# Performance work log

Measured on AMD Instinct MI355X. Metric: run time of the kernel, lower is better.

## Reference

```python
import jax, jax.numpy as jnp
import numpy as np

D = 85  # label-distribution length -> selects A3 branch

def _build_A(d):
    if d == 5:
        base = jnp.arange(5)
        return 1.0 - jnp.abs(base[:, None] - base[None, :]) / 5.0
    if d == 10:
        base = jnp.arange(10)
        return 1.0 - jnp.abs(base[:, None] - base[None, :]) / 10.0
    base = jnp.arange(85)
    return (1.0 - jnp.abs(base[:, None] - base[None, :]) / 85.0).astype(jnp.float32)

def setup_inputs() -> dict:
    key = jax.random.key(0)
    k1, k2 = jax.random.split(key)
    B = 262144
    inp = jax.random.normal(k1, (B, D), dtype=jnp.float32)
    tgt = jax.random.uniform(k2, (B, D), dtype=jnp.float32)
    return {"input": inp, "target": tgt}

def reference(input, target):
    A = _build_A(input.shape[1]).astype(input.dtype)
    diff = jnp.abs(input - target)            # [B, d]
    # per-row quadratic form diff_i^T A diff_i, summed over batch
    q = jnp.einsum('bi,ij,bj->b', diff, A, diff)
    return 0.1 * q.sum()
```

## Files before the change

### kernel.cpp

```cpp
#include <hip/hip_runtime.h>


#define QFD_D 85
#define ROWS_PER_BLOCK 16
#define THREADS 64

#define F4_VALID 340
#define ROUNDS 6
#define BUF_FLOATS (ROUNDS * 256)

typedef __attribute__((address_space(1))) const void glob_cv;
typedef __attribute__((address_space(3))) void lds_v;

__global__ __launch_bounds__(THREADS) void qfd_kernel(
    const float* __restrict__ in, const float* __restrict__ tgt,
    float* __restrict__ partial) {
    __shared__ float lin[BUF_FLOATS];
    __shared__ float ltg[BUF_FLOATS];
    const int lane = threadIdx.x;
    const long base4 = (long)blockIdx.x * F4_VALID;

    const float4* in4 = reinterpret_cast<const float4*>(in) + base4;
    const float4* tg4 = reinterpret_cast<const float4*>(tgt) + base4;

    #pragma unroll
    for (int r = 0; r < ROUNDS; ++r) {
        int idx = r * 64 + lane;
        int g = idx < F4_VALID ? idx : 0;
        __builtin_amdgcn_global_load_lds(
            (glob_cv*)(in4 + g), (lds_v*)&lin[r * 256], 16, 0, 0);
        __builtin_amdgcn_global_load_lds(
            (glob_cv*)(tg4 + g), (lds_v*)&ltg[r * 256], 16, 0, 0);
    }
    __syncthreads();

    const int q   = lane & 3;
    const int row = lane >> 2;
    const int off = 21 * q + (q != 0);
    const int p   = row * QFD_D + off;

    float l = 0.0f, a1 = 0.0f, b2 = 0.0f;
    #pragma unroll
    for (int j = 0; j < 21; ++j) {
        float v = fabsf(lin[p + j] - ltg[p + j]);
        l += v;
        a1 += l;
        b2 = fmaf(l, l, b2);
    }
    if (q == 0) {
        float v = fabsf(lin[p + 21] - ltg[p + 21]);
        l += v;
        a1 += l;
        b2 = fmaf(l, l, b2);
    }

    const int qb = lane & 60;
    float s0 = __shfl(l, qb + 0, 64);
    float s1 = __shfl(l, qb + 1, 64);
    float s2 = __shfl(l, qb + 2, 64);
    float s3 = __shfl(l, qb + 3, 64);
    float S  = (s0 + s1) + (s2 + s3);
    float P  = (q > 0 ? s0 : 0.0f) + (q > 1 ? s1 : 0.0f) + (q > 2 ? s2 : 0.0f);
    float len = (q == 0) ? 22.0f : 21.0f;
    float c1 = fmaf(len, P, a1);
    float c2 = fmaf(len * P, P, fmaf(2.0f * P, a1, b2));
    float c1s = __shfl(c1, qb + 0, 64) + __shfl(c1, qb + 1, 64)
              + __shfl(c1, qb + 2, 64) + __shfl(c1, qb + 3, 64);
    float c2s = __shfl(c2, qb + 0, 64) + __shfl(c2, qb + 1, 64)
              + __shfl(c2, qb + 2, 64) + __shfl(c2, qb + 3, 64);
    float sumL  = c1s - S;
    float sumL2 = c2s - S * S;
    float qrow  = fmaf(S, S, -(2.0f / 85.0f) * (S * sumL - sumL2));
    float val   = (q == 0) ? qrow : 0.0f;

    #pragma unroll
    for (int m = 32; m > 0; m >>= 1)
        val += __shfl_xor(val, m, 64);
    if (lane == 0) partial[blockIdx.x] = val;
}

__global__ __launch_bounds__(256) void qfd_reduce_kernel(
    const float* __restrict__ partial, float* __restrict__ out, int n) {
    __shared__ float wsum[4];
    const int tid = threadIdx.x;
    float s = 0.0f;
    for (int i = tid; i < n; i += 256) s += partial[i];
    #pragma unroll
    for (int m = 32; m > 0; m >>= 1)
        s += __shfl_xor(s, m, 64);
    if ((tid & 63) == 0) wsum[tid >> 6] = s;
    __syncthreads();
    if (tid == 0) {
        float t = 0.0f;
        #pragma unroll
        for (int w = 0; w < 4; ++w) t += wsum[w];
        out[0] = 0.1f * t;
    }
}

extern "C" void kernel_launch(void* const* d_in, const int* in_sizes, int n_in,
                              void* d_out, int out_size, void* d_ws, size_t ws_size,
                              hipStream_t stream) {
    const float* in  = (const float*)d_in[0];
    const float* tgt = (const float*)d_in[1];
    float* out = (float*)d_out;
    float* partial = (float*)d_ws;

    const int B = in_sizes[0] / QFD_D;
    const int grid = B / ROWS_PER_BLOCK;

    qfd_kernel<<<grid, THREADS, 0, stream>>>(in, tgt, partial);
    qfd_reduce_kernel<<<1, 256, 0, stream>>>(partial, out, grid);
}
```

Before: 204.4 us.

## Replace LDS staging with direct register loads and grid-stride wave scans

Drops the global-to-LDS staging and instead has each wave read three 85-float rows straight into registers as unaligned 4-float vectors, with one extra scalar load for the row tail. Per-row prefix sums and the quadratic-form terms are built with full-wave shuffle scans. A fixed grid of 256-thread blocks runs a grid-stride loop over row groups, and a block-level reduction produces the partials. This removes the LDS round trip and the per-block launch overhead of many tiny blocks, at the cost of unaligned vector loads, a wasted lane per wave, and more shuffle work per row.

```diff
diff --git a/kernel.cpp b/kernel.cpp
--- a/kernel.cpp
+++ b/kernel.cpp
@@ -2,81 +2,118 @@
 
 
 #define QFD_D 85
-#define ROWS_PER_BLOCK 16
-#define THREADS 64
+#define THREADS 256
+#define NWAVES (THREADS / 64)
 
-#define F4_VALID 340
-#define ROUNDS 6
-#define BUF_FLOATS (ROUNDS * 256)
+typedef float f4a __attribute__((ext_vector_type(4), aligned(4)));
 
-typedef __attribute__((address_space(1))) const void glob_cv;
-typedef __attribute__((address_space(3))) void lds_v;
+__global__ __launch_bounds__(THREADS, 6) void qfd_kernel(
+    const float* __restrict__ in, const float* __restrict__ tgt,
+    float* __restrict__ partial, int B, int ngroups) {
+    __shared__ float wsum[NWAVES];
+    const int tid  = threadIdx.x;
+    const int lane = tid & 63;
+    const int wave = tid >> 6;
 
-__global__ __launch_bounds__(THREADS) void qfd_kernel(
-    const float* __restrict__ in, const float* __restrict__ tgt,
-    float* __restrict__ partial) {
-    __shared__ float lin[BUF_FLOATS];
-    __shared__ float ltg[BUF_FLOATS];
-    const int lane = threadIdx.x;
-    const long base4 = (long)blockIdx.x * F4_VALID;
+    const int r = (lane < 21) ? 0 : (lane < 42) ? 1 : (lane < 63) ? 2 : 3;
+    const int c = lane - 21 * r;
+    const bool isC20 = (c == 20) && (r < 3);
+    const int limv = B * QFD_D - 4;
+    const int lims = B * QFD_D - 1;
 
-    const float4* in4 = reinterpret_cast<const float4*>(in) + base4;
-    const float4* tg4 = reinterpret_cast<const float4*>(tgt) + base4;
+    const int wid     = blockIdx.x * NWAVES + wave;
+    const int wstride = gridDim.x * NWAVES;
 
-    #pragma unroll
-    for (int r = 0; r < ROUNDS; ++r) {
-        int idx = r * 64 + lane;
-        int g = idx < F4_VALID ? idx : 0;
-        __builtin_amdgcn_global_load_lds(
-            (glob_cv*)(in4 + g), (lds_v*)&lin[r * 256], 16, 0, 0);
-        __builtin_amdgcn_global_load_lds(
-            (glob_cv*)(tg4 + g), (lds_v*)&ltg[r * 256], 16, 0, 0);
+    float acc = 0.0f;
+
+    for (int g = wid; g < ngroups; g += wstride) {
+        const int base = g * 255;
+        const int row  = 3 * g + r;
+        const bool valid = (r < 3) && (row < B);
+
+        int off = base + r * 85 + c * 4;
+        off = off > limv ? limv : off;
+        f4a vi = *(const f4a*)(in  + off);
+        f4a vt = *(const f4a*)(tgt + off);
+
+        float ti = 0.0f, tt = 0.0f;
+        if (isC20) {
+            int toff = base + r * 85 + 84;
+            toff = toff > lims ? lims : toff;
+            ti = in[toff];
+            tt = tgt[toff];
+        }
+
+        float d0 = valid ? fabsf(vi.x - vt.x) : 0.0f;
+        float d1 = valid ? fabsf(vi.y - vt.y) : 0.0f;
+        float d2 = valid ? fabsf(vi.z - vt.z) : 0.0f;
+        float d3 = valid ? fabsf(vi.w - vt.w) : 0.0f;
+
+        float l  = d0;
+        float a1 = l;
+        float b2 = l * l;
+        l += d1; a1 += l; b2 = fmaf(l, l, b2);
+        l += d2; a1 += l; b2 = fmaf(l, l, b2);
+        l += d3; a1 += l; b2 = fmaf(l, l, b2);
+        const bool ct = isC20 && valid;
+        float d4 = ct ? fabsf(ti - tt) : 0.0f;
+        float l5 = l + d4;
+        a1 += ct ? l5 : 0.0f;
+        b2 = ct ? fmaf(l5, l5, b2) : b2;
+        l  = ct ? l5 : l;
+        float s = l;
+
+        float ps = s;
+        #pragma unroll
+        for (int d = 1; d < 64; d <<= 1) {
+            float t = __shfl_up(ps, d, 64);
+            if (lane >= d) ps += t;
+        }
+        float bs1 = __shfl(ps, 20, 64);
+        float bs2 = __shfl(ps, 41, 64);
+        float rowbase = (r == 0) ? 0.0f : (r == 1) ? bs1 : bs2;
+        float P = ps - s - rowbase;
+        float len = ct ? 5.0f : 4.0f;
+        float c1 = fmaf(len, P, a1);
+        float c2 = fmaf(len * P, P, fmaf(2.0f * P, a1, b2));
+
+        float pc1 = c1, pc2 = c2;
+        #pragma unroll
+        for (int d = 1; d < 64; d <<= 1) {
+            float t1 = __shfl_up(pc1, d, 64);
+            float t2 = __shfl_up(pc2, d, 64);
+            if (lane >= d) { pc1 += t1; pc2 += t2; }
+        }
+
+        int rr = (r < 3) ? r : 2;
+        int e  = 21 * rr + 20;
+        float S   = __shfl(ps, e, 64) - ((rr == 0) ? 0.0f : (rr == 1) ? bs1 : bs2);
+        float hi1 = __shfl(pc1, e, 64);
+        float hi2 = __shfl(pc2, e, 64);
+        int lo_lane = (rr == 0) ? 0 : (21 * rr - 1);
+        float lo1 = __shfl(pc1, lo_lane, 64);
+        float lo2 = __shfl(pc2, lo_lane, 64);
+        lo1 = (rr == 0) ? 0.0f : lo1;
+        lo2 = (rr == 0) ? 0.0f : lo2;
+        float c1s = hi1 - lo1;
+        float c2s = hi2 - lo2;
+        float sumL  = c1s - S;
+        float sumL2 = c2s - S * S;
+        float q = fmaf(S, S, -(2.0f / 85.0f) * (S * sumL - sumL2));
+        acc += (c == 0 && r < 3) ? q : 0.0f;
     }
-    __syncthreads();
-
-    const int q   = lane & 3;
-    const int row = lane >> 2;
-    const int off = 21 * q + (q != 0);
-    const int p   = row * QFD_D + off;
-
-    float l = 0.0f, a1 = 0.0f, b2 = 0.0f;
-    #pragma unroll
-    for (int j = 0; j < 21; ++j) {
-        float v = fabsf(lin[p + j] - ltg[p + j]);
-        l += v;
-        a1 += l;
-        b2 = fmaf(l, l, b2);
-    }
-    if (q == 0) {
-        float v = fabsf(lin[p + 21] - ltg[p + 21]);
-        l += v;
-        a1 += l;
-        b2 = fmaf(l, l, b2);
-    }
-
-    const int qb = lane & 60;
-    float s0 = __shfl(l, qb + 0, 64);
-    float s1 = __shfl(l, qb + 1, 64);
-    float s2 = __shfl(l, qb + 2, 64);
-    float s3 = __shfl(l, qb + 3, 64);
-    float S  = (s0 + s1) + (s2 + s3);
-    float P  = (q > 0 ? s0 : 0.0f) + (q > 1 ? s1 : 0.0f) + (q > 2 ? s2 : 0.0f);
-    float len = (q == 0) ? 22.0f : 21.0f;
-    float c1 = fmaf(len, P, a1);
-    float c2 = fmaf(len * P, P, fmaf(2.0f * P, a1, b2));
-    float c1s = __shfl(c1, qb + 0, 64) + __shfl(c1, qb + 1, 64)
-              + __shfl(c1, qb + 2, 64) + __shfl(c1, qb + 3, 64);
-    float c2s = __shfl(c2, qb + 0, 64) + __shfl(c2, qb + 1, 64)
-              + __shfl(c2, qb + 2, 64) + __shfl(c2, qb + 3, 64);
-    float sumL  = c1s - S;
-    float sumL2 = c2s - S * S;
-    float qrow  = fmaf(S, S, -(2.0f / 85.0f) * (S * sumL - sumL2));
-    float val   = (q == 0) ? qrow : 0.0f;
 
     #pragma unroll
     for (int m = 32; m > 0; m >>= 1)
-        val += __shfl_xor(val, m, 64);
-    if (lane == 0) partial[blockIdx.x] = val;
+        acc += __shfl_xor(acc, m, 64);
+    if (lane == 0) wsum[wave] = acc;
+    __syncthreads();
+    if (tid == 0) {
+        float ssum = 0.0f;
+        #pragma unroll
+        for (int w = 0; w < NWAVES; ++w) ssum += wsum[w];
+        partial[blockIdx.x] = ssum;
+    }
 }
 
 __global__ __launch_bounds__(256) void qfd_reduce_kernel(
@@ -107,8 +144,9 @@
     float* partial = (float*)d_ws;
 
     const int B = in_sizes[0] / QFD_D;
-    const int grid = B / ROWS_PER_BLOCK;
+    const int ngroups = (B + 2) / 3;
+    const int grid = 2048;
 
-    qfd_kernel<<<grid, THREADS, 0, stream>>>(in, tgt, partial);
+    qfd_kernel<<<grid, THREADS, 0, stream>>>(in, tgt, partial, B, ngroups);
     qfd_reduce_kernel<<<1, 256, 0, stream>>>(partial, out, grid);
 }
```

Result: faster. 199.8 us (-2.3%).
